# Kernel tuning notes

Hardware: AMD Instinct MI355X
Metric: run time of the kernel (lower is better)

Reference implementation:

```python
import jax, jax.numpy as jnp
import numpy as np

EMB_W, COMMIT_W, ENT_W = 1.0, 0.25, 0.1  # loss weights from init_kwargs


def setup_inputs() -> dict:
    key = jax.random.key(0)
    k1, k2 = jax.random.split(key)
    B, H, W, D, K = 32, 32, 32, 64, 1024
    inputs = jax.random.normal(k1, (B, H, W, D), dtype=jnp.float32)
    # keras RandomUniform default: U(-0.05, 0.05)
    codebook = jax.random.uniform(k2, (K, D), dtype=jnp.float32, minval=-0.05, maxval=0.05)
    return {"inputs": inputs, "codebook": codebook}


def reference(inputs, codebook):
    # inputs: [B,H,W,D], codebook: [K,D]
    D = inputs.shape[-1]
    x = inputs.reshape(-1, D)  # [N,D]
    dist = (
        jnp.sum(x * x, axis=-1, keepdims=True)
        - 2.0 * (x @ codebook.T)
        + jnp.sum(codebook * codebook, axis=-1)
    )  # [N,K]
    tokens = jnp.argmin(dist, axis=-1)  # [N]
    emb = codebook[tokens].reshape(inputs.shape)  # [B,H,W,D]

    embedding_loss = EMB_W * jnp.mean((jax.lax.stop_gradient(emb) - inputs) ** 2)
    commitment_loss = COMMIT_W * jnp.mean((emb - jax.lax.stop_gradient(inputs)) ** 2)
    # 'entropy' loss as written in call(): mean over codebook of per-code min distance
    entropy_loss = ENT_W * jnp.mean(jnp.min(dist, axis=0))
    loss = embedding_loss + commitment_loss + entropy_loss

    # training=True path: straight-through estimator
    out = inputs + jax.lax.stop_gradient(emb - inputs)
    return out, loss
```

## Files before the change

### kernel.cpp

```cpp
#include <hip/hip_runtime.h>
#include <math.h>

#define NROWS 32768
#define NCODE 1024
#define AMB_CAP 8192
#define GAP_THRESH 1.5e-4f

typedef __attribute__((ext_vector_type(8))) short bf16x8;
typedef __attribute__((ext_vector_type(4))) float f32x4;

__device__ __forceinline__ unsigned short bf16_rne(float f) {
    unsigned u = __float_as_uint(f);
    unsigned r = u + 0x7FFFu + ((u >> 16) & 1u);
    return (unsigned short)(r >> 16);
}

typedef const __attribute__((address_space(1))) unsigned GU;
typedef __attribute__((address_space(3))) unsigned LU;
__device__ __forceinline__ void gl_lds16(const void* g, void* l) {
    __builtin_amdgcn_global_load_lds((GU*)g, (LU*)l, 16, 0, 0);
}
__device__ __forceinline__ void gl_lds4(const void* g, void* l) {
    __builtin_amdgcn_global_load_lds((GU*)g, (LU*)l, 4, 0, 0);
}

__global__ __launch_bounds__(64) void vq_prep(
    const float* __restrict__ cb, float* __restrict__ cn4,
    unsigned* __restrict__ minK, unsigned* __restrict__ counter,
    float* __restrict__ gsumsq, unsigned* __restrict__ ticket,
    unsigned short* __restrict__ wsB)
{
    int c = blockIdx.x * 64 + threadIdx.x;
    if (c == 0) { *counter = 0u; *gsumsq = 0.f; *ticket = 0u; }
    float v[64];
    const float4* src = (const float4*)(cb + (size_t)c * 64);
    float s = 0.f;
    #pragma unroll
    for (int i = 0; i < 16; i++) {
        float4 t = src[i];
        v[i*4+0] = t.x; v[i*4+1] = t.y; v[i*4+2] = t.z; v[i*4+3] = t.w;
        s += t.x*t.x + t.y*t.y + t.z*t.z + t.w*t.w;
    }
    cn4[c] = s + 4.0f;
    minK[c] = 0x7F800000u;
    int cc = c >> 6, ct = (c >> 4) & 3, cl = c & 15;
    #pragma unroll
    for (int q = 0; q < 4; q++) {
        int half = q & 1, lo = q >> 1;
        #pragma unroll
        for (int g = 0; g < 4; g++) {
            unsigned short u8[8] __attribute__((aligned(16)));
            #pragma unroll
            for (int j = 0; j < 8; j++) {
                float f = v[half*32 + g*8 + j];
                unsigned short h = bf16_rne(f);
                if (lo) h = bf16_rne(f - __uint_as_float((unsigned)h << 16));
                u8[j] = h;
            }
            size_t off = (size_t)cc * 8192 + ct * 2048 + q * 512 + (g * 16 + cl) * 8;
            *(uint4*)(wsB + off) = *(const uint4*)u8;
        }
    }
}

__global__ __launch_bounds__(512, 4) void vq_main(
    const float* __restrict__ x, const float* __restrict__ cb,
    const unsigned short* __restrict__ wsB, const float* __restrict__ cn4,
    float* __restrict__ out, unsigned* __restrict__ minK,
    unsigned* __restrict__ counter, int* __restrict__ amb,
    float* __restrict__ gsumsq)
{
    __shared__ __align__(16) unsigned char Bb[2][32768];
    __shared__ float cn4L[2][128];
    __shared__ unsigned scrE[1024];
    __shared__ float mD1[128], mD2[128];
    __shared__ int   mI1[128];
    __shared__ int   tokS[64];
    __shared__ float redS[8];

    const int tid = threadIdx.x;
    const int lane = tid & 63;
    const int wi = tid >> 6;
    const int g = wi >> 1;
    const int h = wi & 1;
    const int ln15 = lane & 15;
    const int q = lane >> 4;
    const int row0 = blockIdx.x * 64;
    const int rot = blockIdx.x & 7;

    scrE[tid] = 0x7F800000u;
    scrE[512 + tid] = 0x7F800000u;

    const char* wsBb = (const char*)wsB;
    {
        int wbase = (tid & ~63) * 16;
        #pragma unroll
        for (int i = 0; i < 4; i++)
            gl_lds16(wsBb + (size_t)rot*32768 + (i*512 + tid)*16,
                     (void*)&Bb[0][i*8192 + wbase]);
        if (wi == 0) {
            gl_lds4(cn4 + rot*128 + lane,      (void*)&cn4L[0][0]);
            gl_lds4(cn4 + rot*128 + 64 + lane, (void*)&cn4L[0][64]);
        }
    }

    bf16x8 Ah0, Ah1, Al0, Al1;
    float xnm4[4];
    {
        const float* xr = x + (size_t)(row0 + g*16 + ln15) * 64 + q * 8;
        float4 f0 = *(const float4*)xr;
        float4 f1 = *(const float4*)(xr + 4);
        float4 f2 = *(const float4*)(xr + 32);
        float4 f3 = *(const float4*)(xr + 36);
        float fa[8] = {f0.x,f0.y,f0.z,f0.w,f1.x,f1.y,f1.z,f1.w};
        float fb[8] = {f2.x,f2.y,f2.z,f2.w,f3.x,f3.y,f3.z,f3.w};
        unsigned short hh8[8] __attribute__((aligned(16)));
        unsigned short ll8[8] __attribute__((aligned(16)));
        unsigned short h28[8] __attribute__((aligned(16)));
        unsigned short l28[8] __attribute__((aligned(16)));
        float ss = 0.f;
        #pragma unroll
        for (int j = 0; j < 8; j++) {
            ss += fa[j]*fa[j] + fb[j]*fb[j];
            unsigned short hh = bf16_rne(fa[j]);
            hh8[j] = hh; ll8[j] = bf16_rne(fa[j] - __uint_as_float((unsigned)hh << 16));
            hh = bf16_rne(fb[j]);
            h28[j] = hh; l28[j] = bf16_rne(fb[j] - __uint_as_float((unsigned)hh << 16));
        }
        Ah0 = *(const bf16x8*)hh8; Al0 = *(const bf16x8*)ll8;
        Ah1 = *(const bf16x8*)h28; Al1 = *(const bf16x8*)l28;
        ss += __shfl_xor(ss, 16);
        ss += __shfl_xor(ss, 32);
        #pragma unroll
        for (int r = 0; r < 4; r++)
            xnm4[r] = __shfl(ss, (q << 2) | r, 64) - 4.0f;
    }

    float d1[4], d2[4];
    int   i1[4];
    #pragma unroll
    for (int r = 0; r < 4; r++) { d1[r] = INFINITY; d2[r] = INFINITY; i1[r] = 0; }

    for (int s = 0; s < 8; s++) {
        __syncthreads();
        const int cb_ = s & 1, nb = (s + 1) & 1;
        const int cphys = (s + rot) & 7;
        if (s < 7) {
            const int cnx = (s + 1 + rot) & 7;
            int wbase = (tid & ~63) * 16;
            #pragma unroll
            for (int i = 0; i < 4; i++)
                gl_lds16(wsBb + (size_t)cnx*32768 + (i*512 + tid)*16,
                         (void*)&Bb[nb][i*8192 + wbase]);
            if (wi == 0) {
                gl_lds4(cn4 + cnx*128 + lane,      (void*)&cn4L[nb][0]);
                gl_lds4(cn4 + cnx*128 + 64 + lane, (void*)&cn4L[nb][64]);
            }
        }
        const unsigned char* buf = Bb[cb_];
        #pragma unroll
        for (int lct = 0; lct < 4; lct++) {
            const int ct = 4*h + lct;
            const unsigned char* tb = buf + (ct >> 2)*16384 + (ct & 3)*4096;
            bf16x8 Bh0 = *(const bf16x8*)(tb +    0 + lane*16);
            bf16x8 Bh1 = *(const bf16x8*)(tb + 1024 + lane*16);
            bf16x8 Bl0 = *(const bf16x8*)(tb + 2048 + lane*16);
            bf16x8 Bl1 = *(const bf16x8*)(tb + 3072 + lane*16);
            float cn4v = cn4L[cb_][ct*16 + ln15];
            int kid = cphys*128 + ct*16 + ln15;
            f32x4 z = {0.f, 0.f, 0.f, 0.f};
            f32x4 acc0 = __builtin_amdgcn_mfma_f32_16x16x32_bf16(Ah0, Bh0, z, 0, 0, 0);
            f32x4 acc1 = __builtin_amdgcn_mfma_f32_16x16x32_bf16(Ah1, Bh1, z, 0, 0, 0);
            acc0 = __builtin_amdgcn_mfma_f32_16x16x32_bf16(Ah0, Bl0, acc0, 0, 0, 0);
            acc1 = __builtin_amdgcn_mfma_f32_16x16x32_bf16(Ah1, Bl1, acc1, 0, 0, 0);
            acc0 = __builtin_amdgcn_mfma_f32_16x16x32_bf16(Al0, Bh0, acc0, 0, 0, 0);
            acc1 = __builtin_amdgcn_mfma_f32_16x16x32_bf16(Al1, Bh1, acc1, 0, 0, 0);
            float cminv = INFINITY;
            #pragma unroll
            for (int r = 0; r < 4; r++) {
                float sdot = acc0[r] + acc1[r];
                float wv = fmaf(sdot, -2.0f, cn4v);
                bool lt = wv < d1[r];
                d2[r] = lt ? d1[r] : fminf(d2[r], wv);
                i1[r] = lt ? kid   : i1[r];
                d1[r] = lt ? wv    : d1[r];
                cminv = fminf(cminv, wv + xnm4[r]);
            }
            cminv = fminf(cminv, __shfl_xor(cminv, 16));
            cminv = fminf(cminv, __shfl_xor(cminv, 32));
            if (q == lct) atomicMin(&scrE[kid], __float_as_uint(cminv));
        }
    }
    __syncthreads();

    #pragma unroll
    for (int d = 1; d < 16; d <<= 1) {
        #pragma unroll
        for (int r = 0; r < 4; r++) {
            float od1 = __shfl_xor(d1[r], d);
            int   oi1 = __shfl_xor(i1[r], d);
            float od2 = __shfl_xor(d2[r], d);
            bool take = (od1 < d1[r]) || (od1 == d1[r] && oi1 < i1[r]);
            float loser = take ? d1[r] : od1;
            d2[r] = fminf(fminf(d2[r], od2), loser);
            d1[r] = take ? od1 : d1[r];
            i1[r] = take ? oi1 : i1[r];
        }
    }
    if (ln15 == 0) {
        #pragma unroll
        for (int r = 0; r < 4; r++) {
            int idx = (g*16 + q*4 + r) * 2 + h;
            mD1[idx] = d1[r]; mI1[idx] = i1[r]; mD2[idx] = d2[r];
        }
    }
    __syncthreads();

    if (tid < 64) {
        float a1 = mD1[tid*2],   b1 = mD1[tid*2+1];
        int   ai = mI1[tid*2],   bi = mI1[tid*2+1];
        float a2 = mD2[tid*2],   b2 = mD2[tid*2+1];
        bool ta = (a1 < b1) || (a1 == b1 && ai < bi);
        float D1 = ta ? a1 : b1;
        int   I1 = ta ? ai : bi;
        float D2 = ta ? fminf(a2, b1) : fminf(b2, a1);
        tokS[tid] = I1;
        if (D2 - D1 < GAP_THRESH) {
            unsigned idx = atomicAdd(counter, 1u);
            if (idx < AMB_CAP) { amb[2*idx] = row0 + tid; amb[2*idx+1] = I1; }
        }
    }

    {
        unsigned u0 = scrE[tid];
        if (u0 < minK[tid]) atomicMin(&minK[tid], u0);
        unsigned u1 = scrE[512 + tid];
        if (u1 < minK[512 + tid]) atomicMin(&minK[512 + tid], u1);
    }
    __syncthreads();

    {
        float acc2 = 0.f;
        #pragma unroll
        for (int uu = 0; uu < 2; uu++) {
            int u = uu*512 + tid;
            int row = u >> 4, c4 = u & 15;
            int tok = tokS[row];
            float4 c = ((const float4*)(cb + (size_t)tok*64))[c4];
            float4 xx = ((const float4*)(x + (size_t)(row0 + row)*64))[c4];
            ((float4*)(out + (size_t)(row0 + row)*64))[c4] = c;
            float dx = c.x-xx.x, dy = c.y-xx.y, dz = c.z-xx.z, dw = c.w-xx.w;
            acc2 += dx*dx + dy*dy + dz*dz + dw*dw;
        }
        #pragma unroll
        for (int o = 32; o > 0; o >>= 1) acc2 += __shfl_down(acc2, o);
        if (lane == 0) redS[wi] = acc2;
        __syncthreads();
        if (tid == 0) {
            float t = 0.f;
            #pragma unroll
            for (int w = 0; w < 8; w++) t += redS[w];
            atomicAdd(gsumsq, t);
        }
    }
}

__global__ __launch_bounds__(256) void vq_tail(
    const float* __restrict__ x, const float* __restrict__ cb,
    float* __restrict__ out, const unsigned* __restrict__ counter,
    const int* __restrict__ amb, float* __restrict__ gsumsq,
    unsigned* __restrict__ ticket, const unsigned* __restrict__ minK,
    float* __restrict__ out_loss)
{
    __shared__ double xs[64];
    __shared__ double bd[256];
    __shared__ int    bi[256];
    __shared__ unsigned lastS;
    __shared__ float redS[4];

    const int tid = threadIdx.x;

    unsigned cnt = *counter; if (cnt > AMB_CAP) cnt = AMB_CAP;
    for (unsigned i = blockIdx.x; i < cnt; i += gridDim.x) {
        int row = amb[2*i], oldk = amb[2*i+1];
        __syncthreads();
        if (tid < 64) xs[tid] = (double)x[(size_t)row*64 + tid];
        __syncthreads();
        double xn = 0.0;
        #pragma unroll 8
        for (int d = 0; d < 64; d++) xn += xs[d]*xs[d];
        double best = INFINITY; int bk = 1 << 30;
        #pragma unroll
        for (int j = 0; j < 4; j++) {
            int k = j*256 + tid;
            const float4* c4 = (const float4*)(cb + (size_t)k*64);
            double dot = 0.0, cn2 = 0.0;
            #pragma unroll
            for (int t = 0; t < 16; t++) {
                float4 cv = c4[t];
                double cx = (double)cv.x, cy = (double)cv.y, cz = (double)cv.z, cw = (double)cv.w;
                dot += xs[t*4+0]*cx + xs[t*4+1]*cy + xs[t*4+2]*cz + xs[t*4+3]*cw;
                cn2 += cx*cx + cy*cy + cz*cz + cw*cw;
            }
            double dist = (xn - 2.0*dot) + cn2;
            if (dist < best || (dist == best && k < bk)) { best = dist; bk = k; }
        }
        bd[tid] = best; bi[tid] = bk;
        __syncthreads();
        for (int s = 128; s > 0; s >>= 1) {
            if (tid < s) {
                double od = bd[tid+s]; int ok = bi[tid+s];
                if (od < bd[tid] || (od == bd[tid] && ok < bi[tid])) { bd[tid] = od; bi[tid] = ok; }
            }
            __syncthreads();
        }
        int bestk = bi[0];
        if (bestk != oldk) {
            double part = 0.0;
            if (tid < 64) {
                float cn = cb[(size_t)bestk*64 + tid];
                float co = cb[(size_t)oldk*64 + tid];
                out[(size_t)row*64 + tid] = cn;
                double dn = (double)cn - xs[tid];
                double dl = (double)co - xs[tid];
                part = dn*dn - dl*dl;
            }
            __syncthreads();
            bd[tid] = part;
            __syncthreads();
            for (int s = 128; s > 0; s >>= 1) {
                if (tid < s) bd[tid] += bd[tid+s];
                __syncthreads();
            }
            if (tid == 0) atomicAdd(gsumsq, (float)bd[0]);
        }
    }

    __syncthreads();
    if (tid == 0) {
        __threadfence();
        lastS = (atomicAdd(ticket, 1u) == (unsigned)(gridDim.x - 1)) ? 1u : 0u;
    }
    __syncthreads();
    if (lastS) {
        __threadfence();
        float s = 0.f;
        #pragma unroll
        for (int jj = 0; jj < 4; jj++)
            s += __uint_as_float(minK[jj*256 + tid]);
        #pragma unroll
        for (int o = 32; o > 0; o >>= 1) s += __shfl_down(s, o);
        if ((tid & 63) == 0) redS[tid >> 6] = s;
        __syncthreads();
        if (tid == 0) {
            float gs = atomicAdd(gsumsq, 0.0f);
            float tot = redS[0] + redS[1] + redS[2] + redS[3];
            out_loss[0] = 1.25f * (gs / 2097152.0f) + 0.1f * (tot / 1024.0f);
        }
    }
}

extern "C" void kernel_launch(void* const* d_in, const int* in_sizes, int n_in,
                              void* d_out, int out_size, void* d_ws, size_t ws_size,
                              hipStream_t stream) {
    const float* x  = (const float*)d_in[0];
    const float* cb = (const float*)d_in[1];
    float* out = (float*)d_out;

    char* ws = (char*)d_ws;
    unsigned*       counter = (unsigned*)ws;
    float*          gsumsq  = (float*)(ws + 4);
    unsigned*       ticket  = (unsigned*)(ws + 8);
    float*          cn4     = (float*)(ws + 1024);
    unsigned*       minK    = (unsigned*)(ws + 8192);
    int*            amb     = (int*)(ws + 16384);
    unsigned short* wsB     = (unsigned short*)(ws + 131072);

    vq_prep<<<16,  64,  0, stream>>>(cb, cn4, minK, counter, gsumsq, ticket, wsB);
    vq_main<<<512, 512, 0, stream>>>(x, cb, wsB, cn4, out, minK, counter, amb, gsumsq);
    vq_tail<<<64,  256, 0, stream>>>(x, cb, out, counter, amb, gsumsq, ticket, minK,
                                     out + 2097152);
}
```

Baseline: 128.8 us.

## Fuse codebook bf16 split into main kernel and replace atomics with partial buffers

```diff
diff --git a/kernel.cpp b/kernel.cpp
--- a/kernel.cpp
+++ b/kernel.cpp
@@ -3,8 +3,8 @@
 
 #define NROWS 32768
 #define NCODE 1024
-#define AMB_CAP 8192
 #define GAP_THRESH 1.5e-4f
+#define FLAG_TAG_SHIFT 30
 
 typedef __attribute__((ext_vector_type(8))) short bf16x8;
 typedef __attribute__((ext_vector_type(4))) float f32x4;
@@ -15,60 +15,11 @@
     return (unsigned short)(r >> 16);
 }
 
-typedef const __attribute__((address_space(1))) unsigned GU;
-typedef __attribute__((address_space(3))) unsigned LU;
-__device__ __forceinline__ void gl_lds16(const void* g, void* l) {
-    __builtin_amdgcn_global_load_lds((GU*)g, (LU*)l, 16, 0, 0);
-}
-__device__ __forceinline__ void gl_lds4(const void* g, void* l) {
-    __builtin_amdgcn_global_load_lds((GU*)g, (LU*)l, 4, 0, 0);
-}
-
-__global__ __launch_bounds__(64) void vq_prep(
-    const float* __restrict__ cb, float* __restrict__ cn4,
-    unsigned* __restrict__ minK, unsigned* __restrict__ counter,
-    float* __restrict__ gsumsq, unsigned* __restrict__ ticket,
-    unsigned short* __restrict__ wsB)
-{
-    int c = blockIdx.x * 64 + threadIdx.x;
-    if (c == 0) { *counter = 0u; *gsumsq = 0.f; *ticket = 0u; }
-    float v[64];
-    const float4* src = (const float4*)(cb + (size_t)c * 64);
-    float s = 0.f;
-    #pragma unroll
-    for (int i = 0; i < 16; i++) {
-        float4 t = src[i];
-        v[i*4+0] = t.x; v[i*4+1] = t.y; v[i*4+2] = t.z; v[i*4+3] = t.w;
-        s += t.x*t.x + t.y*t.y + t.z*t.z + t.w*t.w;
-    }
-    cn4[c] = s + 4.0f;
-    minK[c] = 0x7F800000u;
-    int cc = c >> 6, ct = (c >> 4) & 3, cl = c & 15;
-    #pragma unroll
-    for (int q = 0; q < 4; q++) {
-        int half = q & 1, lo = q >> 1;
-        #pragma unroll
-        for (int g = 0; g < 4; g++) {
-            unsigned short u8[8] __attribute__((aligned(16)));
-            #pragma unroll
-            for (int j = 0; j < 8; j++) {
-                float f = v[half*32 + g*8 + j];
-                unsigned short h = bf16_rne(f);
-                if (lo) h = bf16_rne(f - __uint_as_float((unsigned)h << 16));
-                u8[j] = h;
-            }
-            size_t off = (size_t)cc * 8192 + ct * 2048 + q * 512 + (g * 16 + cl) * 8;
-            *(uint4*)(wsB + off) = *(const uint4*)u8;
-        }
-    }
-}
-
 __global__ __launch_bounds__(512, 4) void vq_main(
     const float* __restrict__ x, const float* __restrict__ cb,
-    const unsigned short* __restrict__ wsB, const float* __restrict__ cn4,
-    float* __restrict__ out, unsigned* __restrict__ minK,
-    unsigned* __restrict__ counter, int* __restrict__ amb,
-    float* __restrict__ gsumsq)
+    float* __restrict__ out, float* __restrict__ entPartial,
+    unsigned* __restrict__ flags, float* __restrict__ sumsqP,
+    unsigned* __restrict__ ticket)
 {
     __shared__ __align__(16) unsigned char Bb[2][32768];
     __shared__ float cn4L[2][128];
@@ -88,20 +39,45 @@
     const int row0 = blockIdx.x * 64;
     const int rot = blockIdx.x & 7;
 
+    if (blockIdx.x == 0 && tid == 0) *ticket = 0u;
+
     scrE[tid] = 0x7F800000u;
     scrE[512 + tid] = 0x7F800000u;
 
-    const char* wsBb = (const char*)wsB;
+    auto stage = [&](int bufIdx, float4 v0, float4 v1, float4 v2, float4 v3) {
+        float f[16] = {v0.x,v0.y,v0.z,v0.w, v1.x,v1.y,v1.z,v1.w,
+                       v2.x,v2.y,v2.z,v2.w, v3.x,v3.y,v3.z,v3.w};
+        float ss = 0.f;
+        #pragma unroll
+        for (int j = 0; j < 16; j++) ss = fmaf(f[j], f[j], ss);
+        ss += __shfl_xor(ss, 1);
+        ss += __shfl_xor(ss, 2);
+        const int lc = tid >> 2, p = tid & 3;
+        const int ct = lc >> 4, cl = lc & 15;
+        const int half = p >> 1, gp = p & 1;
+        unsigned char* tb = Bb[bufIdx] + (ct >> 2)*16384 + (ct & 3)*4096;
+        #pragma unroll
+        for (int sub = 0; sub < 2; sub++) {
+            unsigned short h8[8] __attribute__((aligned(16)));
+            unsigned short l8[8] __attribute__((aligned(16)));
+            #pragma unroll
+            for (int j = 0; j < 8; j++) {
+                float ff = f[sub*8 + j];
+                unsigned short hi = bf16_rne(ff);
+                h8[j] = hi;
+                l8[j] = bf16_rne(ff - __uint_as_float((unsigned)hi << 16));
+            }
+            int off = ((gp*2 + sub)*16 + cl) * 16;
+            *(uint4*)(tb + half*1024 + off)        = *(const uint4*)h8;
+            *(uint4*)(tb + 2048 + half*1024 + off) = *(const uint4*)l8;
+        }
+        if (p == 0) cn4L[bufIdx][lc] = ss + 4.0f;
+    };
+
+    float4 v0, v1, v2, v3;
     {
-        int wbase = (tid & ~63) * 16;
-        #pragma unroll
-        for (int i = 0; i < 4; i++)
-            gl_lds16(wsBb + (size_t)rot*32768 + (i*512 + tid)*16,
-                     (void*)&Bb[0][i*8192 + wbase]);
-        if (wi == 0) {
-            gl_lds4(cn4 + rot*128 + lane,      (void*)&cn4L[0][0]);
-            gl_lds4(cn4 + rot*128 + 64 + lane, (void*)&cn4L[0][64]);
-        }
+        const float4* ls = (const float4*)(cb + ((size_t)rot*128 + (tid>>2))*64 + (tid&3)*16);
+        v0 = ls[0]; v1 = ls[1]; v2 = ls[2]; v3 = ls[3];
     }
 
     bf16x8 Ah0, Ah1, Al0, Al1;
@@ -136,6 +112,8 @@
             xnm4[r] = __shfl(ss, (q << 2) | r, 64) - 4.0f;
     }
 
+    stage(0, v0, v1, v2, v3);
+
     float d1[4], d2[4];
     int   i1[4];
     #pragma unroll
@@ -147,15 +125,8 @@
         const int cphys = (s + rot) & 7;
         if (s < 7) {
             const int cnx = (s + 1 + rot) & 7;
-            int wbase = (tid & ~63) * 16;
-            #pragma unroll
-            for (int i = 0; i < 4; i++)
-                gl_lds16(wsBb + (size_t)cnx*32768 + (i*512 + tid)*16,
-                         (void*)&Bb[nb][i*8192 + wbase]);
-            if (wi == 0) {
-                gl_lds4(cn4 + cnx*128 + lane,      (void*)&cn4L[nb][0]);
-                gl_lds4(cn4 + cnx*128 + 64 + lane, (void*)&cn4L[nb][64]);
-            }
+            const float4* ls = (const float4*)(cb + ((size_t)cnx*128 + (tid>>2))*64 + (tid&3)*16);
+            v0 = ls[0]; v1 = ls[1]; v2 = ls[2]; v3 = ls[3];
         }
         const unsigned char* buf = Bb[cb_];
         #pragma unroll
@@ -190,6 +161,7 @@
             cminv = fminf(cminv, __shfl_xor(cminv, 32));
             if (q == lct) atomicMin(&scrE[kid], __float_as_uint(cminv));
         }
+        if (s < 7) stage(nb, v0, v1, v2, v3);
     }
     __syncthreads();
 
@@ -225,18 +197,12 @@
         int   I1 = ta ? ai : bi;
         float D2 = ta ? fminf(a2, b1) : fminf(b2, a1);
         tokS[tid] = I1;
-        if (D2 - D1 < GAP_THRESH) {
-            unsigned idx = atomicAdd(counter, 1u);
-            if (idx < AMB_CAP) { amb[2*idx] = row0 + tid; amb[2*idx+1] = I1; }
-        }
-    }
-
-    {
-        unsigned u0 = scrE[tid];
-        if (u0 < minK[tid]) atomicMin(&minK[tid], u0);
-        unsigned u1 = scrE[512 + tid];
-        if (u1 < minK[512 + tid]) atomicMin(&minK[512 + tid], u1);
-    }
+        if (D2 - D1 < GAP_THRESH)
+            flags[row0 + tid] = (1u << FLAG_TAG_SHIFT) | (unsigned)I1;
+    }
+
+    entPartial[(size_t)blockIdx.x * 1024 + tid]       = __uint_as_float(scrE[tid]);
+    entPartial[(size_t)blockIdx.x * 1024 + 512 + tid] = __uint_as_float(scrE[512 + tid]);
     __syncthreads();
 
     {
@@ -260,29 +226,63 @@
             float t = 0.f;
             #pragma unroll
             for (int w = 0; w < 8; w++) t += redS[w];
-            atomicAdd(gsumsq, t);
+            sumsqP[blockIdx.x] = t;
         }
     }
 }
 
 __global__ __launch_bounds__(256) void vq_tail(
     const float* __restrict__ x, const float* __restrict__ cb,
-    float* __restrict__ out, const unsigned* __restrict__ counter,
-    const int* __restrict__ amb, float* __restrict__ gsumsq,
-    unsigned* __restrict__ ticket, const unsigned* __restrict__ minK,
-    float* __restrict__ out_loss)
+    float* __restrict__ out, const float* __restrict__ entPartial,
+    const unsigned* __restrict__ flags, const float* __restrict__ sumsqP,
+    float* __restrict__ deltaP, float* __restrict__ partial2,
+    unsigned* __restrict__ ticket, float* __restrict__ out_loss)
 {
     __shared__ double xs[64];
     __shared__ double bd[256];
     __shared__ int    bi[256];
+    __shared__ float  scrR[256];
+    __shared__ int    listRow[32], listTok[32];
+    __shared__ int    lcnt;
+    __shared__ double deltaS;
     __shared__ unsigned lastS;
-    __shared__ float redS[4];
+    __shared__ float redS[4], redS2[4];
 
     const int tid = threadIdx.x;
-
-    unsigned cnt = *counter; if (cnt > AMB_CAP) cnt = AMB_CAP;
-    for (unsigned i = blockIdx.x; i < cnt; i += gridDim.x) {
-        int row = amb[2*i], oldk = amb[2*i+1];
+    const int lane = tid & 63;
+    const int w = tid >> 6;
+    const int b = blockIdx.x;
+
+    if (tid == 0) { lcnt = 0; deltaS = 0.0; }
+
+    {
+        int rg = b >> 4, cgp = b & 15;
+        float m = INFINITY;
+        #pragma unroll 8
+        for (int i = 0; i < 32; i++)
+            m = fminf(m, entPartial[(size_t)(rg*128 + w*32 + i)*1024 + cgp*64 + lane]);
+        scrR[w*64 + lane] = m;
+    }
+    __syncthreads();
+    if (w == 0) {
+        float m = fminf(fminf(scrR[lane], scrR[64+lane]),
+                        fminf(scrR[128+lane], scrR[192+lane]));
+        partial2[(size_t)(b >> 4)*1024 + (b & 15)*64 + lane] = m;
+    }
+
+    #pragma unroll
+    for (int u = 0; u < 2; u++) {
+        int row = b*512 + u*256 + tid;
+        unsigned f = flags[row];
+        if ((f >> FLAG_TAG_SHIFT) == 1u) {
+            int idx = atomicAdd(&lcnt, 1);
+            if (idx < 32) { listRow[idx] = row; listTok[idx] = (int)(f & 1023u); }
+        }
+    }
+    __syncthreads();
+    int nfix = lcnt < 32 ? lcnt : 32;
+    for (int i = 0; i < nfix; i++) {
+        int row = listRow[i], oldk = listTok[i];
         __syncthreads();
         if (tid < 64) xs[tid] = (double)x[(size_t)row*64 + tid];
         __syncthreads();
@@ -332,30 +332,38 @@
                 if (tid < s) bd[tid] += bd[tid+s];
                 __syncthreads();
             }
-            if (tid == 0) atomicAdd(gsumsq, (float)bd[0]);
-        }
-    }
+            if (tid == 0) deltaS += bd[0];
+        }
+    }
+    __syncthreads();
+    if (tid == 0) deltaP[b] = (float)deltaS;
 
     __syncthreads();
     if (tid == 0) {
         __threadfence();
-        lastS = (atomicAdd(ticket, 1u) == (unsigned)(gridDim.x - 1)) ? 1u : 0u;
+        lastS = (atomicAdd(ticket, 1u) == 63u) ? 1u : 0u;
     }
     __syncthreads();
     if (lastS) {
         __threadfence();
-        float s = 0.f;
-        #pragma unroll
-        for (int jj = 0; jj < 4; jj++)
-            s += __uint_as_float(minK[jj*256 + tid]);
-        #pragma unroll
-        for (int o = 32; o > 0; o >>= 1) s += __shfl_down(s, o);
-        if ((tid & 63) == 0) redS[tid >> 6] = s;
+        volatile const float* sp = sumsqP;
+        volatile const float* dp = deltaP;
+        volatile const float* p2 = partial2;
+        float sq = sp[tid] + sp[256 + tid] + ((tid < 64) ? dp[tid] : 0.f);
+        float es = 0.f;
+        #pragma unroll
+        for (int jj = 0; jj < 4; jj++) {
+            int c = jj*256 + tid;
+            es += fminf(fminf(p2[c], p2[1024 + c]), fminf(p2[2048 + c], p2[3072 + c]));
+        }
+        #pragma unroll
+        for (int o = 32; o > 0; o >>= 1) { sq += __shfl_down(sq, o); es += __shfl_down(es, o); }
+        if (lane == 0) { redS[w] = sq; redS2[w] = es; }
         __syncthreads();
         if (tid == 0) {
-            float gs = atomicAdd(gsumsq, 0.0f);
-            float tot = redS[0] + redS[1] + redS[2] + redS[3];
-            out_loss[0] = 1.25f * (gs / 2097152.0f) + 0.1f * (tot / 1024.0f);
+            float S = redS[0] + redS[1] + redS[2] + redS[3];
+            float E = redS2[0] + redS2[1] + redS2[2] + redS2[3];
+            out_loss[0] = 1.25f * (S / 2097152.0f) + 0.1f * (E / 1024.0f);
         }
     }
 }
@@ -368,16 +376,14 @@
     float* out = (float*)d_out;
 
     char* ws = (char*)d_ws;
-    unsigned*       counter = (unsigned*)ws;
-    float*          gsumsq  = (float*)(ws + 4);
-    unsigned*       ticket  = (unsigned*)(ws + 8);
-    float*          cn4     = (float*)(ws + 1024);
-    unsigned*       minK    = (unsigned*)(ws + 8192);
-    int*            amb     = (int*)(ws + 16384);
-    unsigned short* wsB     = (unsigned short*)(ws + 131072);
-
-    vq_prep<<<16,  64,  0, stream>>>(cb, cn4, minK, counter, gsumsq, ticket, wsB);
-    vq_main<<<512, 512, 0, stream>>>(x, cb, wsB, cn4, out, minK, counter, amb, gsumsq);
-    vq_tail<<<64,  256, 0, stream>>>(x, cb, out, counter, amb, gsumsq, ticket, minK,
-                                     out + 2097152);
+    unsigned* ticket     = (unsigned*)ws;
+    float*    sumsqP     = (float*)(ws + 1024);
+    float*    deltaP     = (float*)(ws + 4096);
+    unsigned* flags      = (unsigned*)(ws + 8192);
+    float*    partial2   = (float*)(ws + 139264);
+    float*    entPartial = (float*)(ws + 262144);
+
+    vq_main<<<512, 512, 0, stream>>>(x, cb, out, entPartial, flags, sumsqP, ticket);
+    vq_tail<<<64,  256, 0, stream>>>(x, cb, out, entPartial, flags, sumsqP, deltaP,
+                                     partial2, ticket, out + 2097152);
 }
```

Measured after the change: 141.0 us. +9.5%, slower.
